# Kernel optimization log

Hardware: AMD Instinct MI355X
Metric: run time of the kernel (lower is better)

Reference implementation:

```python
import jax, jax.numpy as jnp
import numpy as np

DIM = 768
NUM_HEADS = 12
HEAD_DIM = DIM // NUM_HEADS
SCALE = HEAD_DIM ** -0.5


def setup_inputs() -> dict:
    key = jax.random.key(0)
    k1, k2, k3, k4 = jax.random.split(key, 4)
    B, H, W = 8, 32, 32
    x = jax.random.normal(k1, (B, H, W, DIM), dtype=jnp.float32)
    s = DIM ** -0.5
    w_qkv = jax.random.normal(k2, (DIM, 3 * DIM), dtype=jnp.float32) * s
    w_proj = jax.random.normal(k3, (DIM, DIM), dtype=jnp.float32) * s
    b_proj = jax.random.normal(k4, (DIM,), dtype=jnp.float32) * 0.01
    return {"x": x, "w_qkv": w_qkv, "w_proj": w_proj, "b_proj": b_proj}


def reference(x, w_qkv, w_proj, b_proj):
    B, H, W, C = x.shape
    N = H * W
    qkv = (x.reshape(B, N, C) @ w_qkv).reshape(B, N, 3, NUM_HEADS, HEAD_DIM)
    q, k, v = jnp.moveaxis(qkv, 2, 0)  # each (B, N, h, d)
    # scores: (B, h, N, N)
    attn = jnp.einsum('bnhd,bmhd->bhnm', q * SCALE, k)
    attn = jax.nn.softmax(attn, axis=-1)
    out = jnp.einsum('bhnm,bmhd->bnhd', attn, v).reshape(B, H, W, C)
    return out @ w_proj + b_proj
```

## Files before the change

kernel.cpp:

```cpp
#include <hip/hip_runtime.h>

typedef _Float16 half_t;
typedef __attribute__((ext_vector_type(4))) _Float16 half4;
typedef __attribute__((ext_vector_type(8))) _Float16 half8;
typedef __attribute__((ext_vector_type(4))) float floatx4;

#define MFMA_F16(A,B,C)  __builtin_amdgcn_mfma_f32_16x16x32_f16(A,B,C,0,0,0)

typedef __attribute__((address_space(1))) const void gvoid_t;
typedef __attribute__((address_space(3))) void svoid_t;

__device__ __forceinline__ void async_copy16(const half_t* g, half_t* l) {
    __builtin_amdgcn_global_load_lds((gvoid_t*)g, (svoid_t*)l, 16, 0, 0);
}

__global__ __launch_bounds__(256)
void prep_kernel(const float* __restrict__ x, const float* __restrict__ w_qkv,
                 const float* __restrict__ w_proj, half_t* __restrict__ xh,
                 half_t* __restrict__ wqkvT, half_t* __restrict__ wprojT)
{
    __shared__ half_t tile[64 * 65];
    const int id = blockIdx.x, tid = threadIdx.x;
    if (id < 6144) {
        size_t e = (size_t)id * 1024 + tid * 4;
        float4 f = *(const float4*)(x + e);
        half4 h = { (half_t)f.x, (half_t)f.y, (half_t)f.z, (half_t)f.w };
        *(half4*)(xh + e) = h;
        return;
    }
    const float* src; half_t* dst; int lds, tr0, tc0;
    if (id < 6576) { int t = id - 6144; src = w_qkv; dst = wqkvT; lds = 2304;
                     tr0 = (t / 36) * 64; tc0 = (t % 36) * 64; }
    else           { int t = id - 6576; src = w_proj; dst = wprojT; lds = 768;
                     tr0 = (t / 12) * 64; tc0 = (t % 12) * 64; }
    #pragma unroll
    for (int i = 0; i < 4; i++) {
        int e = tid + i * 256, r = e >> 4, c4 = (e & 15) << 2;
        float4 f = *(const float4*)(src + (size_t)(tr0 + r) * lds + tc0 + c4);
        tile[(c4 + 0) * 65 + r] = (half_t)f.x;
        tile[(c4 + 1) * 65 + r] = (half_t)f.y;
        tile[(c4 + 2) * 65 + r] = (half_t)f.z;
        tile[(c4 + 3) * 65 + r] = (half_t)f.w;
    }
    __syncthreads();
    #pragma unroll
    for (int i = 0; i < 4; i++) {
        int e = tid + i * 256, c = e >> 4, r4 = (e & 15) << 2;
        half4 h = { tile[c * 65 + r4], tile[c * 65 + r4 + 1],
                    tile[c * 65 + r4 + 2], tile[c * 65 + r4 + 3] };
        *(half4*)(dst + (size_t)(tc0 + c) * 768 + tr0 + r4) = h;
    }
}

__global__ __launch_bounds__(256, 2)
void gemm_qkv(const half_t* __restrict__ A, const half_t* __restrict__ Bt,
              half_t* __restrict__ q_ws, half_t* __restrict__ k_ws,
              half_t* __restrict__ v_ws)
{
    __shared__ half_t As[4][128 * 32];
    __shared__ half_t Bs[4][192 * 32];

    const int lin  = blockIdx.x;
    const int xcd  = lin & 7, rest = lin >> 3;
    const int m0 = ((rest / 12) * 8 + xcd) * 128;
    const int n0 = (rest % 12) * 192;

    const int tid  = threadIdx.x;
    const int lane = tid & 63;
    const int w    = tid >> 6;
    const int wm   = w >> 1, wn = w & 1;
    const int quad = lane >> 4, l16 = lane & 15;

    const int b0p = (lane ^ (lane >> 2) ^ (lane >> 4)) & 1;
    const int b1p = ((lane >> 1) ^ (lane >> 3)) & 1;
    const int b2p = ((lane >> 2) ^ (lane >> 4)) & 1;
    const int row_log = ((lane >> 2) & 0xC) | ((lane >> 2) & 2) | b2p;
    const int q_log   = (b1p << 1) | b0p;

    const int foff = ((((l16 << 2) | quad) ^ (l16 & 7)) << 3);

    const half_t* a_src0 = A  + (size_t)(m0 + (w*2+0)*16 + row_log) * 768 + q_log*8;
    const half_t* a_src1 = A  + (size_t)(m0 + (w*2+1)*16 + row_log) * 768 + q_log*8;
    const half_t* b_src0 = Bt + (size_t)(n0 + (w*3+0)*16 + row_log) * 768 + q_log*8;
    const half_t* b_src1 = Bt + (size_t)(n0 + (w*3+1)*16 + row_log) * 768 + q_log*8;
    const half_t* b_src2 = Bt + (size_t)(n0 + (w*3+2)*16 + row_log) * 768 + q_log*8;

    floatx4 acc[4][6];
    #pragma unroll
    for (int i = 0; i < 4; i++)
        #pragma unroll
        for (int j = 0; j < 6; j++) acc[i][j] = (floatx4)0.0f;

    #define STAGE(BUF, KO)                                            \
        do {                                                          \
            async_copy16(a_src0 + (KO), &As[BUF][(w*2+0)*512]);       \
            async_copy16(a_src1 + (KO), &As[BUF][(w*2+1)*512]);       \
            async_copy16(b_src0 + (KO), &Bs[BUF][(w*3+0)*512]);       \
            async_copy16(b_src1 + (KO), &Bs[BUF][(w*3+1)*512]);       \
            async_copy16(b_src2 + (KO), &Bs[BUF][(w*3+2)*512]);       \
        } while (0)

    STAGE(0, 0);
    STAGE(1, 32);

    #pragma unroll 1
    for (int t = 0; t < 24; ++t) {
        const int cur = t & 3;
        if (t < 22) STAGE((t + 2) & 3, (t + 2) * 32);
        if (t < 22)       asm volatile("s_waitcnt vmcnt(10)" ::: "memory");
        else if (t == 22) asm volatile("s_waitcnt vmcnt(5)"  ::: "memory");
        else              asm volatile("s_waitcnt vmcnt(0)"  ::: "memory");
        __builtin_amdgcn_s_barrier();

        half8 a[4], b[6];
        #pragma unroll
        for (int mi = 0; mi < 4; mi++)
            a[mi] = *(const half8*)(&As[cur][(wm*4 + mi) * 512 + foff]);
        #pragma unroll
        for (int ni = 0; ni < 6; ni++)
            b[ni] = *(const half8*)(&Bs[cur][(wn*6 + ni) * 512 + foff]);

        __builtin_amdgcn_s_setprio(1);
        #pragma unroll
        for (int mi = 0; mi < 4; mi++)
            #pragma unroll
            for (int ni = 0; ni < 6; ni++)
                acc[mi][ni] = MFMA_F16(a[mi], b[ni], acc[mi][ni]);
        __builtin_amdgcn_s_setprio(0);
    }
    #undef STAGE

    const int sel  = (n0 >= 1536) ? 2 : (n0 >= 768 ? 1 : 0);
    const int rem0 = n0 - sel * 768;
    const int bb   = m0 >> 10;
    const int t0   = m0 & 1023;
    const int rw   = wm * 64;

    if (sel == 0) {
        #pragma unroll
        for (int mi = 0; mi < 4; mi++)
            #pragma unroll
            for (int ni = 0; ni < 6; ni++) {
                int cb = rem0 + wn*96 + ni*16;
                int hh = cb >> 6;
                int d  = (cb & 63) + l16;
                size_t base = (size_t)(bb * 12 + hh) * 65536;
                int tok = t0 + rw + mi*16 + quad*4;
                half4 hv = { (half_t)(acc[mi][ni][0] * 0.125f),
                             (half_t)(acc[mi][ni][1] * 0.125f),
                             (half_t)(acc[mi][ni][2] * 0.125f),
                             (half_t)(acc[mi][ni][3] * 0.125f) };
                *(half4*)(q_ws + base + (size_t)d * 1024 + tok) = hv;
            }
    } else if (sel == 1) {
        #pragma unroll
        for (int mi = 0; mi < 4; mi++)
            #pragma unroll
            for (int ni = 0; ni < 6; ni++) {
                int cb = rem0 + wn*96 + ni*16;
                int hh = cb >> 6;
                int d  = (cb & 63) + l16;
                size_t base = (size_t)(bb * 12 + hh) * 65536;
                #pragma unroll
                for (int r = 0; r < 4; r++) {
                    int tok = t0 + rw + mi*16 + quad*4 + r;
                    k_ws[base + (size_t)tok * 64 + d] = (half_t)acc[mi][ni][r];
                }
            }
    } else {
        #pragma unroll
        for (int mi = 0; mi < 4; mi++)
            #pragma unroll
            for (int ni = 0; ni < 6; ni++) {
                int cb = rem0 + wn*96 + ni*16;
                int hh = cb >> 6;
                int d  = (cb & 63) + l16;
                size_t base = (size_t)(bb * 12 + hh) * 65536;
                int tokb = t0 + rw + (mi >> 1) * 32;
                int tokp = tokb | (quad << 3) | ((mi & 1) << 2);
                half4 hv = { (half_t)acc[mi][ni][0], (half_t)acc[mi][ni][1],
                             (half_t)acc[mi][ni][2], (half_t)acc[mi][ni][3] };
                *(half4*)(v_ws + base + (size_t)d * 1024 + tokp) = hv;
            }
    }
}

__global__ __launch_bounds__(256, 2)
void gemm_proj(const half_t* __restrict__ A, const half_t* __restrict__ Bt,
               float* __restrict__ Cout, const float* __restrict__ bias)
{
    __shared__ half_t As[128 * 64];
    __shared__ half_t Bs[128 * 64];

    const int lin  = blockIdx.x;
    const int xcd  = lin & 7, rest = lin >> 3;
    const int m0 = ((rest / 6) * 8 + xcd) * 128;
    const int n0 = (rest % 6) * 128;

    const int tid  = threadIdx.x;
    const int lane = tid & 63;
    const int w    = tid >> 6;
    const int wm   = w >> 1, wn = w & 1;
    const int quad = lane >> 4, l16 = lane & 15;
    const int lrow = lane >> 3;
    const int lcc  = (lane & 7) ^ lrow;
    const int xsw  = l16 & 7;

    const half_t* Ag = A  + (size_t)(m0 + w * 32 + lrow) * 768 + lcc * 8;
    const half_t* Bg = Bt + (size_t)(n0 + w * 32 + lrow) * 768 + lcc * 8;

    floatx4 acc[4][4];
    #pragma unroll
    for (int i = 0; i < 4; i++)
        #pragma unroll
        for (int j = 0; j < 4; j++) acc[i][j] = (floatx4)0.0f;

    for (int k0 = 0; k0 < 768; k0 += 64) {
        #pragma unroll
        for (int i = 0; i < 4; i++) {
            async_copy16(Ag + (size_t)(i * 8) * 768 + k0, As + (w * 4 + i) * 512);
            async_copy16(Bg + (size_t)(i * 8) * 768 + k0, Bs + (w * 4 + i) * 512);
        }
        __syncthreads();

        #pragma unroll
        for (int ks = 0; ks < 2; ks++) {
            const int co = (((ks << 2) + quad) ^ xsw) * 8;
            half8 a[4], b[4];
            #pragma unroll
            for (int mi = 0; mi < 4; mi++)
                a[mi] = *(const half8*)(As + (wm * 64 + mi * 16 + l16) * 64 + co);
            #pragma unroll
            for (int ni = 0; ni < 4; ni++)
                b[ni] = *(const half8*)(Bs + (wn * 64 + ni * 16 + l16) * 64 + co);
            #pragma unroll
            for (int mi = 0; mi < 4; mi++)
                #pragma unroll
                for (int ni = 0; ni < 4; ni++)
                    acc[mi][ni] = MFMA_F16(a[mi], b[ni], acc[mi][ni]);
        }
        __syncthreads();
    }

    float bias_v[4];
    #pragma unroll
    for (int ni = 0; ni < 4; ni++)
        bias_v[ni] = bias[n0 + wn * 64 + ni * 16 + l16];
    float* scratch = (w < 2 ? (float*)As : (float*)Bs) + (w & 1) * 1152;
    #pragma unroll
    for (int mi = 0; mi < 4; mi++) {
        #pragma unroll
        for (int ni = 0; ni < 4; ni++)
            #pragma unroll
            for (int r = 0; r < 4; r++)
                scratch[(quad * 4 + r) * 72 + ni * 16 + l16] =
                    acc[mi][ni][r] + bias_v[ni];
        #pragma unroll
        for (int i = 0; i < 4; i++) {
            int f = quad + i * 4;
            float4 v4 = *(const float4*)(scratch + l16 * 72 + f * 4);
            int gm = m0 + wm * 64 + mi * 16 + l16;
            *(float4*)(Cout + (size_t)gm * 768 + n0 + wn * 64 + f * 4) = v4;
        }
    }
}

__global__ __launch_bounds__(256, 3)
void attn_kernel(const half_t* __restrict__ qT, const half_t* __restrict__ k,
                 const half_t* __restrict__ vT, half_t* __restrict__ a_ws)
{
    __shared__ __align__(16) half_t Kb[2][4096];
    __shared__ __align__(16) half_t Vb[2][4096];
    __shared__ __align__(16) half_t Qs[64 * 128];

    const int lin  = blockIdx.x;
    const int xcd  = lin & 7, rest = lin >> 3;
    const int qc   = rest & 7;
    const int bh   = (rest >> 3) * 8 + xcd;

    const int tid  = threadIdx.x;
    const int lane = tid & 63;
    const int w    = tid >> 6;
    const int quad = lane >> 4, l16 = lane & 15;

    const half_t* qg = qT + (size_t)bh * 65536;
    const half_t* kg = k  + (size_t)bh * 65536;
    const half_t* vg = vT + (size_t)bh * 65536;

    const int srow = lane >> 3;
    const int sch  = (lane & 7) ^ srow;

    #pragma unroll
    for (int j = 0; j < 4; j++) {
        int d0 = w * 16 + j * 4;
        async_copy16(qg + (size_t)(d0 + (lane >> 4)) * 1024 + qc * 128 + (lane & 15) * 8,
                     &Qs[d0 * 128]);
    }
    #pragma unroll
    for (int j = 0; j < 2; j++) {
        int row = j * 32 + w * 8;
        async_copy16(kg + (size_t)(row + srow) * 64 + sch * 8, &Kb[0][row * 64]);
        async_copy16(vg + (size_t)(row + srow) * 1024 + sch * 8, &Vb[0][row * 64]);
    }
    __syncthreads();

    half8 qf[2][2];
    #pragma unroll
    for (int T = 0; T < 2; T++)
        #pragma unroll
        for (int ks = 0; ks < 2; ks++)
            #pragma unroll
            for (int j = 0; j < 8; j++)
                qf[T][ks][j] = Qs[(ks * 32 + quad * 8 + j) * 128
                                  + T * 64 + w * 16 + l16];

    floatx4 acc_o[2][4];
    floatx4 lacc[2];
    #pragma unroll
    for (int T = 0; T < 2; T++) {
        lacc[T] = (floatx4)0.0f;
        #pragma unroll
        for (int dt = 0; dt < 4; dt++) acc_o[T][dt] = (floatx4)0.0f;
    }

    const int xsw = l16 & 7;
    const half8 vone = { (half_t)1.0f, (half_t)1.0f, (half_t)1.0f, (half_t)1.0f,
                         (half_t)1.0f, (half_t)1.0f, (half_t)1.0f, (half_t)1.0f };

    for (int kt = 0; kt < 16; kt++) {
        const int cb = kt & 1;
        __syncthreads();
        if (kt < 15) {
            #pragma unroll
            for (int j = 0; j < 2; j++) {
                int row = j * 32 + w * 8;
                async_copy16(kg + (size_t)((kt + 1) * 64 + row + srow) * 64 + sch * 8,
                             &Kb[cb ^ 1][row * 64]);
                async_copy16(vg + (size_t)(row + srow) * 1024 + (kt + 1) * 64 + sch * 8,
                             &Vb[cb ^ 1][row * 64]);
            }
        }
        const half_t* Kc = Kb[cb];
        const half_t* Vc = Vb[cb];

        floatx4 sc[2][4];
        #pragma unroll
        for (int T = 0; T < 2; T++)
            #pragma unroll
            for (int mt = 0; mt < 4; mt++) sc[T][mt] = (floatx4)0.0f;
        #pragma unroll
        for (int ks = 0; ks < 2; ks++)
            #pragma unroll
            for (int mt = 0; mt < 4; mt++) {
                half8 kf = *(const half8*)(Kc + (mt * 16 + l16) * 64
                                              + (((ks << 2) + quad) ^ xsw) * 8);
                sc[0][mt] = MFMA_F16(kf, qf[0][ks], sc[0][mt]);
                sc[1][mt] = MFMA_F16(kf, qf[1][ks], sc[1][mt]);
            }

        half8 pa[2][2];
        #pragma unroll
        for (int T = 0; T < 2; T++)
            #pragma unroll
            for (int g = 0; g < 2; g++) {
                half8 ph;
                #pragma unroll
                for (int r = 0; r < 4; r++) ph[r]     = (half_t)__expf(sc[T][2 * g][r]);
                #pragma unroll
                for (int r = 0; r < 4; r++) ph[4 + r] = (half_t)__expf(sc[T][2 * g + 1][r]);
                pa[T][g] = ph;
            }

        #pragma unroll
        for (int g = 0; g < 2; g++) {
            lacc[0] = MFMA_F16(pa[0][g], vone, lacc[0]);
            lacc[1] = MFMA_F16(pa[1][g], vone, lacc[1]);
            #pragma unroll
            for (int dt = 0; dt < 4; dt++) {
                half8 vb = *(const half8*)(Vc + (dt * 16 + l16) * 64
                                              + ((((g << 2) + quad) ^ xsw) << 3));
                acc_o[0][dt] = MFMA_F16(pa[0][g], vb, acc_o[0][dt]);
                acc_o[1][dt] = MFMA_F16(pa[1][g], vb, acc_o[1][dt]);
            }
        }
    }

    const int b = bh / 12, h = bh - (bh / 12) * 12;
    #pragma unroll
    for (int T = 0; T < 2; T++)
        #pragma unroll
        for (int r = 0; r < 4; r++) {
            float inv = 1.0f / lacc[T][r];
            int n = qc * 128 + T * 64 + w * 16 + quad * 4 + r;
            half_t* op = a_ws + ((size_t)(b * 1024 + n)) * 768 + h * 64;
            #pragma unroll
            for (int dt = 0; dt < 4; dt++)
                op[dt * 16 + l16] = (half_t)(acc_o[T][dt][r] * inv);
        }
}

extern "C" void kernel_launch(void* const* d_in, const int* in_sizes, int n_in,
                              void* d_out, int out_size, void* d_ws, size_t ws_size,
                              hipStream_t stream)
{
    (void)in_sizes; (void)n_in; (void)out_size; (void)ws_size;
    const float* x      = (const float*)d_in[0];
    const float* w_qkv  = (const float*)d_in[1];
    const float* w_proj = (const float*)d_in[2];
    const float* b_proj = (const float*)d_in[3];
    float* out = (float*)d_out;

    half_t* ws     = (half_t*)d_ws;
    half_t* q_ws   = ws;
    half_t* k_ws   = ws + 6291456;
    half_t* v_ws   = ws + 2 * 6291456;
    half_t* xh     = ws + 3 * 6291456;
    half_t* wqkvT  = ws + 4 * 6291456;
    half_t* wprojT = wqkvT + 1769472;
    half_t* a_ws   = xh;

    prep_kernel<<<dim3(6720), dim3(256), 0, stream>>>(x, w_qkv, w_proj, xh, wqkvT, wprojT);
    gemm_qkv<<<dim3(768), dim3(256), 0, stream>>>(xh, wqkvT, q_ws, k_ws, v_ws);
    attn_kernel<<<dim3(768), dim3(256), 0, stream>>>(q_ws, k_ws, v_ws, a_ws);
    gemm_proj<<<dim3(384), dim3(256), 0, stream>>>(a_ws, wprojT, out, b_proj);
}
```

Measured before the change: 181.5 us.

## Load GEMM operands directly from global into registers, drop LDS staging

Both GEMMs stop staging A/B tiles through shared memory. Each wave now loads its MFMA fragments straight from global memory into registers, double-buffered in the QKV GEMM and triple-buffered in the projection GEMM. The projection GEMM also moves to 128x192 tiles with 256 blocks. This removes LDS traffic and barriers but loses operand sharing between waves, so L2 and global traffic go up, the loads are uncoalesced 16-byte row fragments, and register pressure rises.

```diff
diff --git a/kernel.cpp b/kernel.cpp
--- a/kernel.cpp
+++ b/kernel.cpp
@@ -52,14 +52,25 @@
     }
 }
 
+#define MMAC46(SA, SB)                                                     \
+    do {                                                                   \
+        _Pragma("unroll") for (int mi = 0; mi < 4; mi++)                   \
+        _Pragma("unroll") for (int ni = 0; ni < 6; ni++)                   \
+            acc[mi][ni] = MFMA_F16(SA[mi], SB[ni], acc[mi][ni]);           \
+    } while (0)
+
+#define MMAC44(SA, SB)                                                     \
+    do {                                                                   \
+        _Pragma("unroll") for (int mi = 0; mi < 4; mi++)                   \
+        _Pragma("unroll") for (int ni = 0; ni < 4; ni++)                   \
+            acc[mi][ni] = MFMA_F16(SA[mi], SB[ni], acc[mi][ni]);           \
+    } while (0)
+
 __global__ __launch_bounds__(256, 2)
 void gemm_qkv(const half_t* __restrict__ A, const half_t* __restrict__ Bt,
               half_t* __restrict__ q_ws, half_t* __restrict__ k_ws,
               half_t* __restrict__ v_ws)
 {
-    __shared__ half_t As[4][128 * 32];
-    __shared__ half_t Bs[4][192 * 32];
-
     const int lin  = blockIdx.x;
     const int xcd  = lin & 7, rest = lin >> 3;
     const int m0 = ((rest / 12) * 8 + xcd) * 128;
@@ -71,19 +82,8 @@
     const int wm   = w >> 1, wn = w & 1;
     const int quad = lane >> 4, l16 = lane & 15;
 
-    const int b0p = (lane ^ (lane >> 2) ^ (lane >> 4)) & 1;
-    const int b1p = ((lane >> 1) ^ (lane >> 3)) & 1;
-    const int b2p = ((lane >> 2) ^ (lane >> 4)) & 1;
-    const int row_log = ((lane >> 2) & 0xC) | ((lane >> 2) & 2) | b2p;
-    const int q_log   = (b1p << 1) | b0p;
-
-    const int foff = ((((l16 << 2) | quad) ^ (l16 & 7)) << 3);
-
-    const half_t* a_src0 = A  + (size_t)(m0 + (w*2+0)*16 + row_log) * 768 + q_log*8;
-    const half_t* a_src1 = A  + (size_t)(m0 + (w*2+1)*16 + row_log) * 768 + q_log*8;
-    const half_t* b_src0 = Bt + (size_t)(n0 + (w*3+0)*16 + row_log) * 768 + q_log*8;
-    const half_t* b_src1 = Bt + (size_t)(n0 + (w*3+1)*16 + row_log) * 768 + q_log*8;
-    const half_t* b_src2 = Bt + (size_t)(n0 + (w*3+2)*16 + row_log) * 768 + q_log*8;
+    const half_t* Abase = A  + (size_t)(m0 + wm * 64 + l16) * 768 + quad * 8;
+    const half_t* Bbase = Bt + (size_t)(n0 + wn * 96 + l16) * 768 + quad * 8;
 
     floatx4 acc[4][6];
     #pragma unroll
@@ -91,44 +91,24 @@
         #pragma unroll
         for (int j = 0; j < 6; j++) acc[i][j] = (floatx4)0.0f;
 
-    #define STAGE(BUF, KO)                                            \
-        do {                                                          \
-            async_copy16(a_src0 + (KO), &As[BUF][(w*2+0)*512]);       \
-            async_copy16(a_src1 + (KO), &As[BUF][(w*2+1)*512]);       \
-            async_copy16(b_src0 + (KO), &Bs[BUF][(w*3+0)*512]);       \
-            async_copy16(b_src1 + (KO), &Bs[BUF][(w*3+1)*512]);       \
-            async_copy16(b_src2 + (KO), &Bs[BUF][(w*3+2)*512]);       \
+    #define LDX46(SA, SB, KC)                                                  \
+        do {                                                                   \
+            _Pragma("unroll") for (int mi = 0; mi < 4; mi++)                   \
+                SA[mi] = *(const half8*)(Abase + (size_t)mi * 12288 + (KC) * 32); \
+            _Pragma("unroll") for (int ni = 0; ni < 6; ni++)                   \
+                SB[ni] = *(const half8*)(Bbase + (size_t)ni * 12288 + (KC) * 32); \
         } while (0)
 
-    STAGE(0, 0);
-    STAGE(1, 32);
-
-    #pragma unroll 1
-    for (int t = 0; t < 24; ++t) {
-        const int cur = t & 3;
-        if (t < 22) STAGE((t + 2) & 3, (t + 2) * 32);
-        if (t < 22)       asm volatile("s_waitcnt vmcnt(10)" ::: "memory");
-        else if (t == 22) asm volatile("s_waitcnt vmcnt(5)"  ::: "memory");
-        else              asm volatile("s_waitcnt vmcnt(0)"  ::: "memory");
-        __builtin_amdgcn_s_barrier();
-
-        half8 a[4], b[6];
-        #pragma unroll
-        for (int mi = 0; mi < 4; mi++)
-            a[mi] = *(const half8*)(&As[cur][(wm*4 + mi) * 512 + foff]);
-        #pragma unroll
-        for (int ni = 0; ni < 6; ni++)
-            b[ni] = *(const half8*)(&Bs[cur][(wn*6 + ni) * 512 + foff]);
-
-        __builtin_amdgcn_s_setprio(1);
-        #pragma unroll
-        for (int mi = 0; mi < 4; mi++)
-            #pragma unroll
-            for (int ni = 0; ni < 6; ni++)
-                acc[mi][ni] = MFMA_F16(a[mi], b[ni], acc[mi][ni]);
-        __builtin_amdgcn_s_setprio(0);
-    }
-    #undef STAGE
+    half8 aX[4], bX[6], aY[4], bY[6];
+    LDX46(aX, bX, 0);
+    #pragma unroll
+    for (int t = 0; t < 12; ++t) {
+        LDX46(aY, bY, 2 * t + 1);
+        MMAC46(aX, bX);
+        if (t < 11) LDX46(aX, bX, 2 * t + 2);
+        MMAC46(aY, bY);
+    }
+    #undef LDX46
 
     const int sel  = (n0 >= 1536) ? 2 : (n0 >= 768 ? 1 : 0);
     const int rem0 = n0 - sel * 768;
@@ -189,78 +169,69 @@
 void gemm_proj(const half_t* __restrict__ A, const half_t* __restrict__ Bt,
                float* __restrict__ Cout, const float* __restrict__ bias)
 {
-    __shared__ half_t As[128 * 64];
-    __shared__ half_t Bs[128 * 64];
+    __shared__ float escr[4][1600];
 
     const int lin  = blockIdx.x;
     const int xcd  = lin & 7, rest = lin >> 3;
-    const int m0 = ((rest / 6) * 8 + xcd) * 128;
-    const int n0 = (rest % 6) * 128;
+    const int m0 = ((rest / 4) * 8 + xcd) * 128;
+    const int n0 = (rest % 4) * 192;
 
     const int tid  = threadIdx.x;
     const int lane = tid & 63;
     const int w    = tid >> 6;
     const int wm   = w >> 1, wn = w & 1;
     const int quad = lane >> 4, l16 = lane & 15;
-    const int lrow = lane >> 3;
-    const int lcc  = (lane & 7) ^ lrow;
-    const int xsw  = l16 & 7;
-
-    const half_t* Ag = A  + (size_t)(m0 + w * 32 + lrow) * 768 + lcc * 8;
-    const half_t* Bg = Bt + (size_t)(n0 + w * 32 + lrow) * 768 + lcc * 8;
-
-    floatx4 acc[4][4];
+
+    const half_t* Abase = A  + (size_t)(m0 + wm * 64 + l16) * 768 + quad * 8;
+    const half_t* Bbase = Bt + (size_t)(n0 + wn * 96 + l16) * 768 + quad * 8;
+
+    floatx4 acc[4][6];
     #pragma unroll
     for (int i = 0; i < 4; i++)
         #pragma unroll
-        for (int j = 0; j < 4; j++) acc[i][j] = (floatx4)0.0f;
-
-    for (int k0 = 0; k0 < 768; k0 += 64) {
-        #pragma unroll
-        for (int i = 0; i < 4; i++) {
-            async_copy16(Ag + (size_t)(i * 8) * 768 + k0, As + (w * 4 + i) * 512);
-            async_copy16(Bg + (size_t)(i * 8) * 768 + k0, Bs + (w * 4 + i) * 512);
-        }
-        __syncthreads();
-
-        #pragma unroll
-        for (int ks = 0; ks < 2; ks++) {
-            const int co = (((ks << 2) + quad) ^ xsw) * 8;
-            half8 a[4], b[4];
-            #pragma unroll
-            for (int mi = 0; mi < 4; mi++)
-                a[mi] = *(const half8*)(As + (wm * 64 + mi * 16 + l16) * 64 + co);
-            #pragma unroll
-            for (int ni = 0; ni < 4; ni++)
-                b[ni] = *(const half8*)(Bs + (wn * 64 + ni * 16 + l16) * 64 + co);
-            #pragma unroll
-            for (int mi = 0; mi < 4; mi++)
-                #pragma unroll
-                for (int ni = 0; ni < 4; ni++)
-                    acc[mi][ni] = MFMA_F16(a[mi], b[ni], acc[mi][ni]);
-        }
-        __syncthreads();
-    }
-
-    float bias_v[4];
-    #pragma unroll
-    for (int ni = 0; ni < 4; ni++)
-        bias_v[ni] = bias[n0 + wn * 64 + ni * 16 + l16];
-    float* scratch = (w < 2 ? (float*)As : (float*)Bs) + (w & 1) * 1152;
+        for (int j = 0; j < 6; j++) acc[i][j] = (floatx4)0.0f;
+
+    #define LDP(SA, SB, KC)                                                    \
+        do {                                                                   \
+            _Pragma("unroll") for (int mi = 0; mi < 4; mi++)                   \
+                SA[mi] = *(const half8*)(Abase + (size_t)mi * 12288 + (KC) * 32); \
+            _Pragma("unroll") for (int ni = 0; ni < 6; ni++)                   \
+                SB[ni] = *(const half8*)(Bbase + (size_t)ni * 12288 + (KC) * 32); \
+        } while (0)
+
+    half8 aX[4], bX[6], aY[4], bY[6], aZ[4], bZ[6];
+    LDP(aX, bX, 0);
+    LDP(aY, bY, 1);
+    #pragma unroll
+    for (int t = 0; t < 8; ++t) {
+        LDP(aZ, bZ, 3 * t + 2);
+        MMAC46(aX, bX);
+        if (3 * t + 3 < 24) LDP(aX, bX, 3 * t + 3);
+        MMAC46(aY, bY);
+        if (3 * t + 4 < 24) LDP(aY, bY, 3 * t + 4);
+        MMAC46(aZ, bZ);
+    }
+    #undef LDP
+
+    float bias_v[6];
+    #pragma unroll
+    for (int ni = 0; ni < 6; ni++)
+        bias_v[ni] = bias[n0 + wn * 96 + ni * 16 + l16];
+    float* scratch = escr[w];
     #pragma unroll
     for (int mi = 0; mi < 4; mi++) {
         #pragma unroll
-        for (int ni = 0; ni < 4; ni++)
+        for (int ni = 0; ni < 6; ni++)
             #pragma unroll
             for (int r = 0; r < 4; r++)
-                scratch[(quad * 4 + r) * 72 + ni * 16 + l16] =
+                scratch[(quad * 4 + r) * 100 + ni * 16 + l16] =
                     acc[mi][ni][r] + bias_v[ni];
         #pragma unroll
-        for (int i = 0; i < 4; i++) {
+        for (int i = 0; i < 6; i++) {
             int f = quad + i * 4;
-            float4 v4 = *(const float4*)(scratch + l16 * 72 + f * 4);
+            float4 v4 = *(const float4*)(scratch + l16 * 100 + f * 4);
             int gm = m0 + wm * 64 + mi * 16 + l16;
-            *(float4*)(Cout + (size_t)gm * 768 + n0 + wn * 64 + f * 4) = v4;
+            *(float4*)(Cout + (size_t)gm * 768 + n0 + wn * 96 + f * 4) = v4;
         }
     }
 }
@@ -422,5 +393,5 @@
     prep_kernel<<<dim3(6720), dim3(256), 0, stream>>>(x, w_qkv, w_proj, xh, wqkvT, wprojT);
     gemm_qkv<<<dim3(768), dim3(256), 0, stream>>>(xh, wqkvT, q_ws, k_ws, v_ws);
     attn_kernel<<<dim3(768), dim3(256), 0, stream>>>(q_ws, k_ws, v_ws, a_ws);
-    gemm_proj<<<dim3(384), dim3(256), 0, stream>>>(a_ws, wprojT, out, b_proj);
-}
+    gemm_proj<<<dim3(256), dim3(256), 0, stream>>>(a_ws, wprojT, out, b_proj);
+}
```

Result: slower. 264.2 us (+45.6%).

## Interleave async LDS prefetch and fragment reads with MFMA in four sub-phases

Applied to the files above, without the earlier changes.

Splits each K-step of the QKV GEMM main loop into four phases. Each phase issues one slice of the next-stage global-to-LDS DMA, reads a subset of A/B fragments from LDS, and runs a 2x3 block of MFMAs, with barriers and sched_barrier keeping the phases in that order. The vmcnt wait moves to the end of the iteration. The goal is to overlap memory traffic and LDS reads with matrix math instead of doing all loads before all MFMAs. The trade-off is several extra barriers per iteration and tighter ordering constraints on the scheduler.

```diff
diff --git a/kernel.cpp b/kernel.cpp
--- a/kernel.cpp
+++ b/kernel.cpp
@@ -91,44 +91,92 @@
         #pragma unroll
         for (int j = 0; j < 6; j++) acc[i][j] = (floatx4)0.0f;
 
-    #define STAGE(BUF, KO)                                            \
-        do {                                                          \
-            async_copy16(a_src0 + (KO), &As[BUF][(w*2+0)*512]);       \
-            async_copy16(a_src1 + (KO), &As[BUF][(w*2+1)*512]);       \
-            async_copy16(b_src0 + (KO), &Bs[BUF][(w*3+0)*512]);       \
-            async_copy16(b_src1 + (KO), &Bs[BUF][(w*3+1)*512]);       \
-            async_copy16(b_src2 + (KO), &Bs[BUF][(w*3+2)*512]);       \
-        } while (0)
-
-    STAGE(0, 0);
-    STAGE(1, 32);
+    #define DMA_A0(BUF, KO) async_copy16(a_src0 + (KO), &As[BUF][(w*2+0)*512])
+    #define DMA_A1(BUF, KO) async_copy16(a_src1 + (KO), &As[BUF][(w*2+1)*512])
+    #define DMA_B0(BUF, KO) async_copy16(b_src0 + (KO), &Bs[BUF][(w*3+0)*512])
+    #define DMA_B1(BUF, KO) async_copy16(b_src1 + (KO), &Bs[BUF][(w*3+1)*512])
+    #define DMA_B2(BUF, KO) async_copy16(b_src2 + (KO), &Bs[BUF][(w*3+2)*512])
+
+    DMA_A0(0, 0); DMA_A1(0, 0); DMA_B0(0, 0); DMA_B1(0, 0); DMA_B2(0, 0);
+    DMA_A0(1, 32); DMA_A1(1, 32); DMA_B0(1, 32); DMA_B1(1, 32); DMA_B2(1, 32);
+    asm volatile("s_waitcnt vmcnt(5)" ::: "memory");
+    __builtin_amdgcn_s_barrier();
 
     #pragma unroll 1
     for (int t = 0; t < 24; ++t) {
         const int cur = t & 3;
-        if (t < 22) STAGE((t + 2) & 3, (t + 2) * 32);
-        if (t < 22)       asm volatile("s_waitcnt vmcnt(10)" ::: "memory");
-        else if (t == 22) asm volatile("s_waitcnt vmcnt(5)"  ::: "memory");
-        else              asm volatile("s_waitcnt vmcnt(0)"  ::: "memory");
-        __builtin_amdgcn_s_barrier();
-
+        const int nxt = (t + 2) & 3;
+        const int ko  = (t + 2) * 32;
+        const bool pf = (t < 22);
         half8 a[4], b[6];
-        #pragma unroll
-        for (int mi = 0; mi < 4; mi++)
-            a[mi] = *(const half8*)(&As[cur][(wm*4 + mi) * 512 + foff]);
-        #pragma unroll
-        for (int ni = 0; ni < 6; ni++)
-            b[ni] = *(const half8*)(&Bs[cur][(wn*6 + ni) * 512 + foff]);
-
+
+        if (pf) { DMA_A0(nxt, ko); DMA_A1(nxt, ko); }
+        a[0] = *(const half8*)(&As[cur][(wm*4 + 0) * 512 + foff]);
+        a[1] = *(const half8*)(&As[cur][(wm*4 + 1) * 512 + foff]);
+        b[0] = *(const half8*)(&Bs[cur][(wn*6 + 0) * 512 + foff]);
+        b[1] = *(const half8*)(&Bs[cur][(wn*6 + 1) * 512 + foff]);
+        b[2] = *(const half8*)(&Bs[cur][(wn*6 + 2) * 512 + foff]);
+        __builtin_amdgcn_s_barrier();
+        asm volatile("s_waitcnt lgkmcnt(0)" ::: "memory");
+        __builtin_amdgcn_sched_barrier(0);
         __builtin_amdgcn_s_setprio(1);
         #pragma unroll
-        for (int mi = 0; mi < 4; mi++)
-            #pragma unroll
-            for (int ni = 0; ni < 6; ni++)
+        for (int mi = 0; mi < 2; mi++)
+            #pragma unroll
+            for (int ni = 0; ni < 3; ni++)
                 acc[mi][ni] = MFMA_F16(a[mi], b[ni], acc[mi][ni]);
         __builtin_amdgcn_s_setprio(0);
-    }
-    #undef STAGE
+        __builtin_amdgcn_s_barrier();
+
+        if (pf) DMA_B0(nxt, ko);
+        b[3] = *(const half8*)(&Bs[cur][(wn*6 + 3) * 512 + foff]);
+        b[4] = *(const half8*)(&Bs[cur][(wn*6 + 4) * 512 + foff]);
+        b[5] = *(const half8*)(&Bs[cur][(wn*6 + 5) * 512 + foff]);
+        __builtin_amdgcn_s_barrier();
+        asm volatile("s_waitcnt lgkmcnt(0)" ::: "memory");
+        __builtin_amdgcn_sched_barrier(0);
+        __builtin_amdgcn_s_setprio(1);
+        #pragma unroll
+        for (int mi = 0; mi < 2; mi++)
+            #pragma unroll
+            for (int ni = 3; ni < 6; ni++)
+                acc[mi][ni] = MFMA_F16(a[mi], b[ni], acc[mi][ni]);
+        __builtin_amdgcn_s_setprio(0);
+        __builtin_amdgcn_s_barrier();
+
+        if (pf) DMA_B1(nxt, ko);
+        a[2] = *(const half8*)(&As[cur][(wm*4 + 2) * 512 + foff]);
+        a[3] = *(const half8*)(&As[cur][(wm*4 + 3) * 512 + foff]);
+        __builtin_amdgcn_s_barrier();
+        asm volatile("s_waitcnt lgkmcnt(0)" ::: "memory");
+        __builtin_amdgcn_sched_barrier(0);
+        __builtin_amdgcn_s_setprio(1);
+        #pragma unroll
+        for (int mi = 2; mi < 4; mi++)
+            #pragma unroll
+            for (int ni = 0; ni < 3; ni++)
+                acc[mi][ni] = MFMA_F16(a[mi], b[ni], acc[mi][ni]);
+        __builtin_amdgcn_s_setprio(0);
+        __builtin_amdgcn_s_barrier();
+
+        if (pf) DMA_B2(nxt, ko);
+        __builtin_amdgcn_s_setprio(1);
+        #pragma unroll
+        for (int mi = 2; mi < 4; mi++)
+            #pragma unroll
+            for (int ni = 3; ni < 6; ni++)
+                acc[mi][ni] = MFMA_F16(a[mi], b[ni], acc[mi][ni]);
+        __builtin_amdgcn_s_setprio(0);
+
+        if (t < 22)       asm volatile("s_waitcnt vmcnt(5)" ::: "memory");
+        else if (t == 22) asm volatile("s_waitcnt vmcnt(0)" ::: "memory");
+        if (t < 23) __builtin_amdgcn_s_barrier();
+    }
+    #undef DMA_A0
+    #undef DMA_A1
+    #undef DMA_B0
+    #undef DMA_B1
+    #undef DMA_B2
 
     const int sel  = (n0 >= 1536) ? 2 : (n0 >= 768 ? 1 : 0);
     const int rem0 = n0 - sel * 768;
```

After: 198.9 us. 9.6% more time.
